# Kernel tuning notes

Hardware: AMD Instinct MI355X
Metric: run time of the kernel (lower is better)

Reference implementation:

```python
import jax, jax.numpy as jnp
import numpy as np

D_MODEL = 1024
N_HEADS = 16
D_HEAD = D_MODEL // N_HEADS
WINDOW = 64
SCALE = 1.0 / np.sqrt(D_HEAD)


def setup_inputs() -> dict:
    key = jax.random.key(0)
    k1, k2, k3 = jax.random.split(key, 3)
    B, N = 1, 4096
    x = jax.random.normal(k1, (B, N, D_MODEL), dtype=jnp.float32)
    # xavier-uniform-ish init for weights (scaled normal is fine for a numeric reference)
    w_qkv = jax.random.normal(k2, (3 * D_MODEL, D_MODEL), dtype=jnp.float32) * (1.0 / np.sqrt(D_MODEL))
    b_qkv = jnp.zeros((3 * D_MODEL,), dtype=jnp.float32)
    w_out = jax.random.normal(k3, (D_MODEL, D_MODEL), dtype=jnp.float32) * (1.0 / np.sqrt(D_MODEL))
    b_out = jnp.zeros((D_MODEL,), dtype=jnp.float32)
    return {"x": x, "w_qkv": w_qkv, "b_qkv": b_qkv, "w_out": w_out, "b_out": b_out}


def reference(x, w_qkv, b_qkv, w_out, b_out):
    B, N, D = x.shape
    # QKV projection (torch Linear: x @ W^T + b)
    qkv = x @ w_qkv.T + b_qkv                      # [B, N, 3D]
    qkv = qkv.reshape(B, N, 3, N_HEADS, D_HEAD)
    qkv = jnp.transpose(qkv, (2, 0, 3, 1, 4))       # [3, B, H, N, dh]
    q, k, v = qkv[0], qkv[1], qkv[2]
    # dense scores, masked to causal sliding window (faithful to original)
    scores = jnp.einsum('bhqd,bhkd->bhqk', q, k) * SCALE  # [B, H, N, N]
    qpos = jnp.arange(N)[:, None]
    kpos = jnp.arange(N)[None, :]
    diff = qpos - kpos
    mask = (diff >= 0) & (diff < WINDOW)            # [N, N]
    scores = jnp.where(mask[None, None, :, :], scores, -jnp.inf)
    attn = jax.nn.softmax(scores, axis=-1)          # every query has >=1 valid key (self)
    out = jnp.einsum('bhqk,bhkd->bhqd', attn, v)    # [B, H, N, dh]
    out = jnp.transpose(out, (0, 2, 1, 3)).reshape(B, N, D)
    out = out @ w_out.T + b_out
    return out
```

## Files before the change

kernel.cpp:

```cpp
#include <hip/hip_runtime.h>
#include <hip/hip_bf16.h>
#include <stdint.h>
#include <stddef.h>

#define NSEQ  4096
#define DM    1024
#define NHEAD 16
#define DHEAD 64
#define WIN   64

using short8 = __attribute__((ext_vector_type(8))) short;
using f32x4  = __attribute__((ext_vector_type(4))) float;

#define GLOBAL_AS __attribute__((address_space(1)))
#define LDS_AS    __attribute__((address_space(3)))

__device__ __forceinline__ unsigned short f2bf(float f) {
  union { float f; unsigned int u; } v; v.f = f;
  unsigned int r = v.u + 0x7FFFu + ((v.u >> 16) & 1u);
  return (unsigned short)(r >> 16);
}

__device__ __forceinline__ void gload_lds16(void* lds, const void* g) {
  __builtin_amdgcn_global_load_lds((const GLOBAL_AS unsigned int*)g,
                                   (LDS_AS unsigned int*)lds, 16, 0, 0);
}

#define NX4 1048576
#define NW4 786432
__global__ void cvt_all(const float* __restrict__ x,
                        const float* __restrict__ wqkv,
                        const float* __restrict__ wout,
                        unsigned short* __restrict__ dst) {
  int i = blockIdx.x * blockDim.x + threadIdx.x;
  float4 f;
  if (i < NX4)            f = ((const float4*)x)[i];
  else if (i < NX4 + NW4) f = ((const float4*)wqkv)[i - NX4];
  else                    f = ((const float4*)wout)[i - (NX4 + NW4)];
  ushort4 o;
  o.x = f2bf(f.x); o.y = f2bf(f.y); o.z = f2bf(f.z); o.w = f2bf(f.w);
  ((ushort4*)dst)[i] = o;
}

__global__ __launch_bounds__(512, 1)
void gemm_qkv(const unsigned short* __restrict__ A,
              const unsigned short* __restrict__ B,
              const float* __restrict__ bias,
              unsigned short* __restrict__ qo,
              unsigned short* __restrict__ ko,
              unsigned short* __restrict__ vo) {
  __shared__ short lds[57344];

  const int bm = blockIdx.x >> 4;
  const int bn = blockIdx.x & 15;
  const int m0 = bm << 8, n0 = bn * 192;
  const int tid = threadIdx.x, w = tid >> 6, l = tid & 63;
  const int wr = w >> 2, wc = w & 3;
  const int l15 = l & 15, l4 = l >> 4;
  const int srow = l >> 2;
  const int skel = ((l & 3) << 3) ^ ((l >= 32) << 4);
  const int roff = l15 * 32 + ((l4 * 8) ^ ((l15 >= 8) * 16));

  f32x4 acc[8][3] = {};

  auto stageA = [&](int j, int qm) {
    const int base = (j & 1) * 28672 + qm * 8192;
#pragma unroll
    for (int r = 0; r < 2; ++r) {
      const int c = r * 8 + w;
      gload_lds16(&lds[base + c * 512 + l * 8],
                  A + (size_t)(m0 + qm * 128 + (c >> 1) * 16 + srow) * 1024
                    + (j << 6) + (c & 1) * 32 + skel);
    }
  };
  auto stageB = [&](int j, int qk) {
    const int base = (j & 1) * 28672 + 16384 + qk * 6144;
    {
      const int c = w;
      gload_lds16(&lds[base + c * 512 + l * 8],
                  B + (size_t)(n0 + c * 16 + srow) * 1024
                    + (j << 6) + qk * 32 + skel);
    }
    {
      const int c = 8 + (w & 3);
      gload_lds16(&lds[base + c * 512 + l * 8],
                  B + (size_t)(n0 + c * 16 + srow) * 1024
                    + (j << 6) + qk * 32 + skel);
    }
  };

  stageA(0, 0); stageA(0, 1); stageB(0, 1); stageB(0, 0); stageB(1, 0);
  asm volatile("s_waitcnt vmcnt(2)" ::: "memory");
  __builtin_amdgcn_s_barrier();

  const int NT = 16;
  for (int j = 0; j < NT; ++j) {
    const int buf = (j & 1) * 28672;
    const short* Ah = &lds[buf + wr * 8192];
#pragma unroll
    for (int p = 0; p < 4; ++p) {
      const int qm = p & 1, qk = p >> 1;
      const short* Bh = &lds[buf + 16384 + qk * 6144];
      short8 af[4], bf[3];
#pragma unroll
      for (int i = 0; i < 4; ++i)
        af[i] = *(const short8*)&Ah[(qm * 4 + i) * 1024 + qk * 512 + roff];
#pragma unroll
      for (int ni = 0; ni < 3; ++ni)
        bf[ni] = *(const short8*)&Bh[(wc * 3 + ni) * 512 + roff];
      if (p == 0 && j + 1 < NT) { stageA(j + 1, 0); stageA(j + 1, 1); stageB(j + 1, 1); }
      if (p == 2 && j + 2 < NT) { stageB(j + 2, 0); }
      if (p == 3) {
        if (j + 2 < NT) asm volatile("s_waitcnt vmcnt(2)" ::: "memory");
        else            asm volatile("s_waitcnt vmcnt(0)" ::: "memory");
      } else {
        asm volatile("" ::: "memory");
      }
      __builtin_amdgcn_s_barrier();
      __builtin_amdgcn_s_setprio(1);
#pragma unroll
      for (int i = 0; i < 4; ++i)
#pragma unroll
        for (int ni = 0; ni < 3; ++ni)
          acc[qm * 4 + i][ni] = __builtin_amdgcn_mfma_f32_16x16x32_bf16(
              af[i], bf[ni], acc[qm * 4 + i][ni], 0, 0, 0);
      __builtin_amdgcn_s_setprio(0);
    }
  }

#pragma unroll
  for (int ni = 0; ni < 3; ++ni) {
    const int n  = n0 + wc * 48 + ni * 16 + l15;
    const float bv = bias[n];
    const int region = n >> 10;
#pragma unroll
    for (int mi = 0; mi < 8; ++mi) {
      const int mb = m0 + wr * 128 + mi * 16 + l4 * 4;
      if (region == 0) {
        const int h = (n >> 6) & 15, d = n & 63;
#pragma unroll
        for (int r = 0; r < 4; ++r)
          qo[((size_t)(h * NSEQ + mb + r)) * DHEAD + d] =
              f2bf((acc[mi][ni][r] + bv) * 0.125f);
      } else if (region == 1) {
        const int nn = n - 1024;
        const int h = nn >> 6, d = nn & 63;
#pragma unroll
        for (int r = 0; r < 4; ++r)
          ko[((size_t)(h * NSEQ + mb + r)) * DHEAD + d] =
              f2bf(acc[mi][ni][r] + bv);
      } else {
        const int nn = n - 2048;
        ushort4 pk;
        pk.x = f2bf(acc[mi][ni][0] + bv);
        pk.y = f2bf(acc[mi][ni][1] + bv);
        pk.z = f2bf(acc[mi][ni][2] + bv);
        pk.w = f2bf(acc[mi][ni][3] + bv);
        *(ushort4*)&vo[(size_t)nn * NSEQ + mb] = pk;
      }
    }
  }
}

__global__ __launch_bounds__(256)
void gemm_op(const unsigned short* __restrict__ A,
             const unsigned short* __restrict__ B,
             const float* __restrict__ bias,
             float* __restrict__ Cf) {
  __shared__ short lds[2][8192];

  const int bm = blockIdx.x >> 4;
  const int bn = blockIdx.x & 15;
  const int m0 = bm << 6, n0 = bn << 6;
  const int tid = threadIdx.x, w = tid >> 6, l = tid & 63;
  const int wr = w >> 1, wc = w & 1;
  const int l15 = l & 15, l4 = l >> 4;
  const int srow = l >> 2;
  const int skel = ((l & 3) << 3) ^ ((l >= 32) << 4);
  const int roff = l15 * 32 + ((l4 * 8) ^ ((l15 >= 8) * 16));

  f32x4 acc[2][2] = {};
  const int NT = 16;

  auto stage = [&](int t) {
    const int buf = t & 1;
    const int kb  = t << 6;
#pragma unroll
    for (int r = 0; r < 2; ++r) {
      const int c = r * 4 + w;
      gload_lds16(&lds[buf][c * 512 + l * 8],
                  A + (size_t)(m0 + (c >> 1) * 16 + srow) * 1024
                    + kb + (c & 1) * 32 + skel);
      gload_lds16(&lds[buf][4096 + c * 512 + l * 8],
                  B + (size_t)(n0 + (c >> 1) * 16 + srow) * 1024
                    + kb + (c & 1) * 32 + skel);
    }
  };

  stage(0);
  for (int t = 0; t < NT; ++t) {
    __syncthreads();
    if (t + 1 < NT) stage(t + 1);
    const short* Ab = &lds[t & 1][0];
    const short* Bb = &lds[t & 1][4096];
    short8 af[2][2], bf[2][2];
#pragma unroll
    for (int mi = 0; mi < 2; ++mi)
#pragma unroll
      for (int kk = 0; kk < 2; ++kk)
        af[mi][kk] = *(const short8*)&Ab[((wr * 2 + mi) * 2 + kk) * 512 + roff];
#pragma unroll
    for (int ni = 0; ni < 2; ++ni)
#pragma unroll
      for (int kk = 0; kk < 2; ++kk)
        bf[ni][kk] = *(const short8*)&Bb[((wc * 2 + ni) * 2 + kk) * 512 + roff];
    __builtin_amdgcn_s_setprio(1);
#pragma unroll
    for (int kk = 0; kk < 2; ++kk)
#pragma unroll
      for (int mi = 0; mi < 2; ++mi)
#pragma unroll
        for (int ni = 0; ni < 2; ++ni)
          acc[mi][ni] = __builtin_amdgcn_mfma_f32_16x16x32_bf16(
              af[mi][kk], bf[ni][kk], acc[mi][ni], 0, 0, 0);
    __builtin_amdgcn_s_setprio(0);
  }

#pragma unroll
  for (int ni = 0; ni < 2; ++ni) {
    const int n  = n0 + wc * 32 + ni * 16 + l15;
    const float bv = bias[n];
#pragma unroll
    for (int mi = 0; mi < 2; ++mi) {
      const int mb = m0 + wr * 32 + mi * 16 + l4 * 4;
#pragma unroll
      for (int r = 0; r < 4; ++r)
        Cf[(size_t)(mb + r) * DM + n] = acc[mi][ni][r] + bv;
    }
  }
}

__global__ __launch_bounds__(256)
void attn_kernel(const unsigned short* __restrict__ Qb,
                 const unsigned short* __restrict__ Kb,
                 const unsigned short* __restrict__ Vt,
                 unsigned short* __restrict__ att) {
  __shared__ short Pl[4][16][136];
  const int h  = blockIdx.x >> 6;
  const int q0 = (blockIdx.x & 63) << 6;
  const int w  = threadIdx.x >> 6;
  const int l  = threadIdx.x & 63;
  const int l15 = l & 15, l4 = l >> 4;
  const int qw = q0 + w * 16;
  const int tb = w & ~1;

  const unsigned short* Qh = Qb + (size_t)h * NSEQ * DHEAD;
  const unsigned short* Kh = Kb + (size_t)h * NSEQ * DHEAD;
  const unsigned short* Vh = Vt + (size_t)h * DHEAD * NSEQ;

  short8 aq[2];
  {
    const int qrow = qw + l15;
    aq[0] = *(const short8*)&Qh[(size_t)qrow * DHEAD + l4 * 8];
    aq[1] = *(const short8*)&Qh[(size_t)qrow * DHEAD + 32 + l4 * 8];
  }

  f32x4 s[6] = {};
#pragma unroll
  for (int tt = 0; tt < 6; ++tt) {
    int j  = q0 - 64 + (tb + tt) * 16 + l15;
    int jc = j < 0 ? 0 : j;
    short8 b0 = *(const short8*)&Kh[(size_t)jc * DHEAD + l4 * 8];
    short8 b1 = *(const short8*)&Kh[(size_t)jc * DHEAD + 32 + l4 * 8];
    s[tt] = __builtin_amdgcn_mfma_f32_16x16x32_bf16(aq[0], b0, s[tt], 0, 0, 0);
    s[tt] = __builtin_amdgcn_mfma_f32_16x16x32_bf16(aq[1], b1, s[tt], 0, 0, 0);
  }

  float rmax[4] = {-3e38f, -3e38f, -3e38f, -3e38f};
#pragma unroll
  for (int tt = 0; tt < 6; ++tt)
#pragma unroll
    for (int r = 0; r < 4; ++r) {
      const int i = qw + l4 * 4 + r;
      const int j = q0 - 64 + (tb + tt) * 16 + l15;
      const int diff = i - j;
      float sv = (j >= 0 && diff >= 0 && diff < WIN) ? s[tt][r] : -3e38f;
      s[tt][r] = sv;
      rmax[r] = fmaxf(rmax[r], sv);
    }
#pragma unroll
  for (int r = 0; r < 4; ++r)
#pragma unroll
    for (int m = 1; m < 16; m <<= 1)
      rmax[r] = fmaxf(rmax[r], __shfl_xor(rmax[r], m, 64));

  float rsum[4] = {0.f, 0.f, 0.f, 0.f};
#pragma unroll
  for (int tt = 0; tt < 6; ++tt)
#pragma unroll
    for (int r = 0; r < 4; ++r) {
      float p = __expf(s[tt][r] - rmax[r]);
      s[tt][r] = p;
      rsum[r] += p;
    }
#pragma unroll
  for (int r = 0; r < 4; ++r)
#pragma unroll
    for (int m = 1; m < 16; m <<= 1)
      rsum[r] += __shfl_xor(rsum[r], m, 64);

#pragma unroll
  for (int tt = 0; tt < 6; ++tt)
#pragma unroll
    for (int r = 0; r < 4; ++r)
      Pl[w][l4 * 4 + r][(tb + tt) * 16 + l15] = (short)f2bf(s[tt][r]);

  f32x4 o[4] = {};
#pragma unroll
  for (int kq = 0; kq < 3; ++kq) {
    const int ks = (w >> 1) + kq;
    short8 ap = *(const short8*)&Pl[w][l15][ks * 32 + l4 * 8];
    int jg = q0 - 64 + ks * 32 + l4 * 8;
    if (jg < 0) jg = 0;
#pragma unroll
    for (int dt = 0; dt < 4; ++dt) {
      const int d = dt * 16 + l15;
      short8 bv = *(const short8*)&Vh[(size_t)d * NSEQ + jg];
      o[dt] = __builtin_amdgcn_mfma_f32_16x16x32_bf16(ap, bv, o[dt], 0, 0, 0);
    }
  }

#pragma unroll
  for (int r = 0; r < 4; ++r) {
    const float rinv = 1.0f / rsum[r];
    const int m = qw + l4 * 4 + r;
#pragma unroll
    for (int dt = 0; dt < 4; ++dt)
      att[(size_t)m * DM + h * DHEAD + dt * 16 + l15] = f2bf(o[dt][r] * rinv);
  }
}

extern "C" void kernel_launch(void* const* d_in, const int* in_sizes, int n_in,
                              void* d_out, int out_size, void* d_ws, size_t ws_size,
                              hipStream_t stream) {
  const float* x    = (const float*)d_in[0];
  const float* wqkv = (const float*)d_in[1];
  const float* bqkv = (const float*)d_in[2];
  const float* wout = (const float*)d_in[3];
  const float* bout = (const float*)d_in[4];
  float* out = (float*)d_out;

  unsigned short* ws = (unsigned short*)d_ws;
  unsigned short* xb    = ws;
  unsigned short* wqkvb = xb    + (size_t)NSEQ * DM;
  unsigned short* woutb = wqkvb + (size_t)3 * DM * DM;
  unsigned short* qb    = woutb + (size_t)DM * DM;
  unsigned short* kb    = qb    + (size_t)NSEQ * DM;
  unsigned short* vtb   = kb    + (size_t)NSEQ * DM;
  unsigned short* attb  = vtb   + (size_t)NSEQ * DM;

  cvt_all<<<8192, 256, 0, stream>>>(x, wqkv, wout, xb);

  gemm_qkv<<<16 * 16, 512, 0, stream>>>(xb, wqkvb, bqkv, qb, kb, vtb);

  attn_kernel<<<NHEAD * (NSEQ / 64), 256, 0, stream>>>(qb, kb, vtb, attb);

  gemm_op<<<64 * 16, 256, 0, stream>>>(attb, woutb, bout, out);
}
```

Measured before the change: 82.19 us.

## Restructure QKV GEMM main loop into explicit ping-pong phased schedule

Rewrites the K-loop of the QKV projection GEMM into four explicit phases. Each phase issues its LDS fragment reads and one quarter of the next tile's global-to-LDS staging, then waits on vmcnt/lgkmcnt behind a barrier and a sched_barrier before a 12-MFMA block. Prefetch distance drops from two B-stages ahead to one tile ahead, and B fragments are reused across the qm halves instead of reloaded. The goal is tighter control of overlap between memory and matrix ops. The cost is roughly twice as many barriers, and a real risk of exposed load latency or hazards from the new wait counts.

```diff
diff --git a/kernel.cpp b/kernel.cpp
--- a/kernel.cpp
+++ b/kernel.cpp
@@ -89,43 +89,71 @@
     }
   };
 
-  stageA(0, 0); stageA(0, 1); stageB(0, 1); stageB(0, 0); stageB(1, 0);
-  asm volatile("s_waitcnt vmcnt(2)" ::: "memory");
+  auto ldA = [&](short8* af, int buf, int qm, int qk) {
+    const short* Ah = &lds[buf + wr * 8192];
+#pragma unroll
+    for (int i = 0; i < 4; ++i)
+      af[i] = *(const short8*)&Ah[(qm * 4 + i) * 1024 + qk * 512 + roff];
+  };
+  auto ldB = [&](short8* bf, int buf, int qk) {
+    const short* Bh = &lds[buf + 16384 + qk * 6144];
+#pragma unroll
+    for (int ni = 0; ni < 3; ++ni)
+      bf[ni] = *(const short8*)&Bh[(wc * 3 + ni) * 512 + roff];
+  };
+  auto mfma12 = [&](const short8* af, const short8* bf, int qm) {
+    __builtin_amdgcn_s_setprio(1);
+#pragma unroll
+    for (int i = 0; i < 4; ++i)
+#pragma unroll
+      for (int ni = 0; ni < 3; ++ni)
+        acc[qm * 4 + i][ni] = __builtin_amdgcn_mfma_f32_16x16x32_bf16(
+            af[i], bf[ni], acc[qm * 4 + i][ni], 0, 0, 0);
+    __builtin_amdgcn_s_setprio(0);
+  };
+
+  stageA(0, 0); stageB(0, 0); stageA(0, 1); stageB(0, 1);
+  asm volatile("s_waitcnt vmcnt(4)" ::: "memory");
   __builtin_amdgcn_s_barrier();
 
   const int NT = 16;
+  short8 af[4], bf[3];
   for (int j = 0; j < NT; ++j) {
     const int buf = (j & 1) * 28672;
-    const short* Ah = &lds[buf + wr * 8192];
-#pragma unroll
-    for (int p = 0; p < 4; ++p) {
-      const int qm = p & 1, qk = p >> 1;
-      const short* Bh = &lds[buf + 16384 + qk * 6144];
-      short8 af[4], bf[3];
-#pragma unroll
-      for (int i = 0; i < 4; ++i)
-        af[i] = *(const short8*)&Ah[(qm * 4 + i) * 1024 + qk * 512 + roff];
-#pragma unroll
-      for (int ni = 0; ni < 3; ++ni)
-        bf[ni] = *(const short8*)&Bh[(wc * 3 + ni) * 512 + roff];
-      if (p == 0 && j + 1 < NT) { stageA(j + 1, 0); stageA(j + 1, 1); stageB(j + 1, 1); }
-      if (p == 2 && j + 2 < NT) { stageB(j + 2, 0); }
-      if (p == 3) {
-        if (j + 2 < NT) asm volatile("s_waitcnt vmcnt(2)" ::: "memory");
-        else            asm volatile("s_waitcnt vmcnt(0)" ::: "memory");
-      } else {
-        asm volatile("" ::: "memory");
-      }
-      __builtin_amdgcn_s_barrier();
-      __builtin_amdgcn_s_setprio(1);
-#pragma unroll
-      for (int i = 0; i < 4; ++i)
-#pragma unroll
-        for (int ni = 0; ni < 3; ++ni)
-          acc[qm * 4 + i][ni] = __builtin_amdgcn_mfma_f32_16x16x32_bf16(
-              af[i], bf[ni], acc[qm * 4 + i][ni], 0, 0, 0);
-      __builtin_amdgcn_s_setprio(0);
-    }
+    const bool st = (j + 1 < NT);
+    ldA(af, buf, 0, 0); ldB(bf, buf, 0);
+    if (st) { stageA(j + 1, 0);
+              asm volatile("s_waitcnt vmcnt(4)" ::: "memory"); }
+    else    { asm volatile("s_waitcnt vmcnt(2)" ::: "memory"); }
+    __builtin_amdgcn_s_barrier();
+    asm volatile("s_waitcnt lgkmcnt(0)" ::: "memory");
+    __builtin_amdgcn_sched_barrier(0);
+    mfma12(af, bf, 0);
+    __builtin_amdgcn_s_barrier();
+    ldA(af, buf, 1, 0);
+    if (st) { stageB(j + 1, 0);
+              asm volatile("s_waitcnt vmcnt(4)" ::: "memory"); }
+    else    { asm volatile("s_waitcnt vmcnt(0)" ::: "memory"); }
+    __builtin_amdgcn_s_barrier();
+    asm volatile("s_waitcnt lgkmcnt(0)" ::: "memory");
+    __builtin_amdgcn_sched_barrier(0);
+    mfma12(af, bf, 1);
+    __builtin_amdgcn_s_barrier();
+    ldA(af, buf, 0, 1); ldB(bf, buf, 1);
+    if (st) stageA(j + 1, 1);
+    __builtin_amdgcn_s_barrier();
+    asm volatile("s_waitcnt lgkmcnt(0)" ::: "memory");
+    __builtin_amdgcn_sched_barrier(0);
+    mfma12(af, bf, 0);
+    __builtin_amdgcn_s_barrier();
+    ldA(af, buf, 1, 1);
+    if (st) { stageB(j + 1, 1);
+              asm volatile("s_waitcnt vmcnt(4)" ::: "memory"); }
+    __builtin_amdgcn_s_barrier();
+    asm volatile("s_waitcnt lgkmcnt(0)" ::: "memory");
+    __builtin_amdgcn_sched_barrier(0);
+    mfma12(af, bf, 1);
+    __builtin_amdgcn_s_barrier();
   }
 
 #pragma unroll
```

Result: no change. 81.38 us (-1.0%).
